# Kernel optimization log

Hardware: AMD Instinct MI355X
Metric: run time of the kernel (lower is better)

The kernel has to match this reference:

```python
import jax, jax.numpy as jnp
import numpy as np

DECAY = 0.8
EPS = 1e-05


def setup_inputs() -> dict:
    key = jax.random.key(0)
    k_x, k_e = jax.random.split(key)
    x = jax.random.normal(k_x, (8, 4096, 256), dtype=jnp.float32)
    embed = jax.random.normal(k_e, (8192, 256), dtype=jnp.float32)
    cluster_size = jnp.zeros((8192,), dtype=jnp.float32)
    embed_avg = embed  # buffer initialized as embed.clone()
    return {"x": x, "embed": embed, "cluster_size": cluster_size, "embed_avg": embed_avg}


def reference(x, embed, cluster_size, embed_avg):
    shape = x.shape
    K, d = embed.shape
    flatten = x.reshape(-1, d)  # [N, d]

    dist = -(jnp.sum(flatten * flatten, axis=1, keepdims=True)
             - 2.0 * (flatten @ embed.T)
             + jnp.sum(embed * embed, axis=1)[None, :])  # [N, K]
    embed_ind = jnp.argmax(dist, axis=-1)  # [N]

    quantize = jnp.take(embed, embed_ind, axis=0).reshape(shape)
    embed_ind_out = embed_ind.reshape(shape[:-1])

    # Training-mode EMA update (one_hot sum / one_hot matmul expressed as scatter-adds)
    counts = jnp.zeros((K,), dtype=x.dtype).at[embed_ind].add(1.0)  # embed_onehot.sum(0)
    embed_sum = jnp.zeros((K, d), dtype=x.dtype).at[embed_ind].add(flatten)  # (flatten^T @ onehot)^T

    new_cluster_size = cluster_size * DECAY + counts * (1.0 - DECAY)
    new_embed_avg = embed_avg * DECAY + embed_sum * (1.0 - DECAY)

    smoothed = (new_cluster_size + EPS) / (new_cluster_size.sum() + K * EPS) * new_cluster_size.sum()
    new_embed = new_embed_avg / smoothed[:, None]

    return quantize, embed_ind_out, new_cluster_size, new_embed_avg, new_embed
```

## Files before the change

### kernel.cpp

```cpp
#include <hip/hip_runtime.h>

#define N_ROWS 32768
#define DIM    256
#define KCODES 8192
#define DECAYF 0.8f
#define OMDF   0.2f
#define EPSF   1e-5f

#define Q_OFF    0
#define IND_OFF  8388608
#define CS_OFF   8421376
#define EA_OFF   8429568
#define NE_OFF   10526720


#define WS_E2    0
#define WS_CNT   8192
#define WS_START 16384
#define WS_CUR   24576
#define WS_SUM   40960

typedef _Float16 half8 __attribute__((ext_vector_type(8)));
typedef float floatx16 __attribute__((ext_vector_type(16)));

#define GLOAD16(g, l) __builtin_amdgcn_global_load_lds( \
    (const __attribute__((address_space(1))) void*)(g), \
    (__attribute__((address_space(3))) void*)(l), 16, 0, 0)

#define PREP_ROWS 32
__global__ void prep_all_kernel(const float* __restrict__ x,
                                const float* __restrict__ embed,
                                const float* __restrict__ cs,
                                _Float16* __restrict__ Xp,
                                _Float16* __restrict__ Ep,
                                float* __restrict__ out,
                                float* __restrict__ ws) {
  __shared__ __align__(16) _Float16 L[PREP_ROWS][264];
  __shared__ float red[4];
  const int t = threadIdx.x;
  const int bid = blockIdx.x;

  if (bid < 1024) {
    if (bid < 128) {
      unsigned long long* gbest = (unsigned long long*)(out + EA_OFF);
      gbest[bid * 256 + t] = 0ULL;
    } else if (bid < 160) {
      ((int*)(ws + WS_CNT))[(bid - 128) * 256 + t] = 0;
    }
    const int row0 = bid * PREP_ROWS;
    #pragma unroll
    for (int it = 0; it < 8; ++it) {
      int idx = it * 256 + t;
      int r = idx >> 6, q = idx & 63;
      float4 v = *(const float4*)&x[(size_t)(row0 + r) * DIM + q * 4];
      L[r][q * 4 + 0] = (_Float16)v.x;
      L[r][q * 4 + 1] = (_Float16)v.y;
      L[r][q * 4 + 2] = (_Float16)v.z;
      L[r][q * 4 + 3] = (_Float16)v.w;
    }
    __syncthreads();
    #pragma unroll
    for (int it = 0; it < 4; ++it) {
      int idx = it * 256 + t;
      int slot = idx >> 5, r = idx & 31;
      *(float4*)&Xp[((size_t)slot * N_ROWS + row0 + r) * 8] =
          *(const float4*)&L[r][slot * 8];
    }
  } else {
    const int row0 = (bid - 1024) * PREP_ROWS;
    float* e2 = ws + WS_E2;
    #pragma unroll
    for (int it = 0; it < 8; ++it) {
      int idx = it * 256 + t;
      int r = idx >> 6, q = idx & 63;
      float4 v = *(const float4*)&embed[(size_t)(row0 + r) * DIM + q * 4];
      L[r][q * 4 + 0] = (_Float16)v.x;
      L[r][q * 4 + 1] = (_Float16)v.y;
      L[r][q * 4 + 2] = (_Float16)v.z;
      L[r][q * 4 + 3] = (_Float16)v.w;
      float ssq = v.x * v.x + v.y * v.y + v.z * v.z + v.w * v.w;
      #pragma unroll
      for (int o = 32; o; o >>= 1) ssq += __shfl_xor(ssq, o);
      if ((t & 63) == 0) e2[row0 + r] = ssq;
    }
    if (bid == 1024) {
      float s = 0.0f;
      for (int j = t; j < KCODES; j += 256) s += cs[j];
      #pragma unroll
      for (int o = 32; o; o >>= 1) s += __shfl_xor(s, o);
      if ((t & 63) == 0) red[t >> 6] = s;
    }
    __syncthreads();
    if (bid == 1024 && t == 0)
      ws[WS_SUM] = red[0] + red[1] + red[2] + red[3];
    #pragma unroll
    for (int it = 0; it < 4; ++it) {
      int idx = it * 256 + t;
      int slot = idx >> 5, r = idx & 31;
      *(float4*)&Ep[((size_t)slot * KCODES + row0 + r) * 8] =
          *(const float4*)&L[r][slot * 8];
    }
  }
}

__global__ __launch_bounds__(512, 2) void main_kernel(
    const _Float16* __restrict__ Xp, const _Float16* __restrict__ Ep,
    const float* __restrict__ e2, unsigned long long* __restrict__ gbest) {
  __shared__ __align__(16) _Float16 As[4 * 4 * 256 * 8];
  __shared__ __align__(16) _Float16 Bs[4 * 4 * 256 * 8];
  __shared__ __align__(16) float e2s[256];

  const int t = threadIdx.x;
  const int w = t >> 6;
  const int lane = t & 63;
  const int l31 = lane & 31;
  const int h = lane >> 5;
  const int wm = w >> 2;
  const int wn = w & 3;

  const int bid = blockIdx.x;
  const int bi = bid >> 3;
  const int cb = (bid & 7) * 4 + (bi >> 3);
  const int rbg = bi & 7;
  const int codes0 = cb * 256;
  const int rowbase = rbg * 4096;

  const bool isA = (w < 4);
  const int slot = isA ? w : (w - 4);

  const _Float16* estage = Ep + ((size_t)slot * KCODES + codes0 + lane) * 8;
  const _Float16* xstage = Xp + ((size_t)slot * N_ROWS + rowbase + lane) * 8;
  _Float16* adst = &As[slot * 2048];
  _Float16* bdst = &Bs[slot * 2048];

  auto stage = [&](int buf, int se4, int rowT) {
    if (isA) {
      const _Float16* src = estage + (size_t)se4 * (KCODES * 8);
      _Float16* dst = adst + buf * 8192;
      #pragma unroll
      for (int q = 0; q < 4; ++q)
        GLOAD16(src + q * 512, dst + q * 512);
    } else {
      const _Float16* src =
          xstage + (size_t)se4 * (N_ROWS * 8) + (size_t)rowT * 2048;
      _Float16* dst = bdst + buf * 8192;
      #pragma unroll
      for (int q = 0; q < 4; ++q)
        GLOAD16(src + q * 512, dst + q * 512);
    }
  };

  if (t < 64) {
    float4 v = *(const float4*)&e2[codes0 + t * 4];
    *(float4*)&e2s[t * 4] = v;
  }
  __builtin_amdgcn_sched_barrier(0);
  stage(0, 0, 0);
  stage(1, 4, 0);
  asm volatile("s_waitcnt vmcnt(4)" ::: "memory");
  asm volatile("s_waitcnt lgkmcnt(0)" ::: "memory");
  __builtin_amdgcn_s_barrier();
  __builtin_amdgcn_sched_barrier(0);

  floatx16 acc[4][2];
  unsigned long long pbest[4][2];

  #pragma unroll 1
  for (int sg = 0; sg < 4; ++sg) {
    #pragma unroll
    for (int tt = 0; tt < 4; ++tt) {
      const int rowT = sg * 4 + tt;
      #pragma unroll
      for (int ct = 0; ct < 4; ++ct) {
        const int cl = wm * 128 + ct * 32 + 4 * h;
        #pragma unroll
        for (int rq = 0; rq < 4; ++rq) {
          float4 v = *(const float4*)&e2s[cl + rq * 8];
          acc[ct][0][rq * 4 + 0] = -0.5f * v.x;
          acc[ct][0][rq * 4 + 1] = -0.5f * v.y;
          acc[ct][0][rq * 4 + 2] = -0.5f * v.z;
          acc[ct][0][rq * 4 + 3] = -0.5f * v.w;
        }
        acc[ct][1] = acc[ct][0];
      }

      #pragma unroll
      for (int i = 0; i < 8; ++i) {
        const bool lastTile = (sg == 3 && tt == 3);
        if (!(lastTile && i >= 6)) {
          const int ip = i + 2;
          stage(ip & 3, (ip & 7) * 4, rowT + (ip >> 3));
        }
        __builtin_amdgcn_sched_barrier(0);

        const int cur = (i & 3) * 8192;
        #pragma unroll
        for (int ks = 0; ks < 2; ++ks) {
          const int sbase = cur + (2 * ks + h) * 2048;
          half8 a0 = *(const half8*)&As[sbase + (wm * 128 + l31) * 8];
          half8 a1 = *(const half8*)&As[sbase + (wm * 128 + 32 + l31) * 8];
          half8 a2 = *(const half8*)&As[sbase + (wm * 128 + 64 + l31) * 8];
          half8 a3 = *(const half8*)&As[sbase + (wm * 128 + 96 + l31) * 8];
          half8 b0 = *(const half8*)&Bs[sbase + (wn * 64 + l31) * 8];
          half8 b1 = *(const half8*)&Bs[sbase + (wn * 64 + 32 + l31) * 8];
          __builtin_amdgcn_s_setprio(1);
          acc[0][0] = __builtin_amdgcn_mfma_f32_32x32x16_f16(a0, b0, acc[0][0], 0, 0, 0);
          acc[0][1] = __builtin_amdgcn_mfma_f32_32x32x16_f16(a0, b1, acc[0][1], 0, 0, 0);
          acc[1][0] = __builtin_amdgcn_mfma_f32_32x32x16_f16(a1, b0, acc[1][0], 0, 0, 0);
          acc[1][1] = __builtin_amdgcn_mfma_f32_32x32x16_f16(a1, b1, acc[1][1], 0, 0, 0);
          acc[2][0] = __builtin_amdgcn_mfma_f32_32x32x16_f16(a2, b0, acc[2][0], 0, 0, 0);
          acc[2][1] = __builtin_amdgcn_mfma_f32_32x32x16_f16(a2, b1, acc[2][1], 0, 0, 0);
          acc[3][0] = __builtin_amdgcn_mfma_f32_32x32x16_f16(a3, b0, acc[3][0], 0, 0, 0);
          acc[3][1] = __builtin_amdgcn_mfma_f32_32x32x16_f16(a3, b1, acc[3][1], 0, 0, 0);
          __builtin_amdgcn_s_setprio(0);
        }
        __builtin_amdgcn_sched_barrier(0);

        if (!(lastTile && i == 7)) {
          if (!(lastTile && i == 6)) {
            asm volatile("s_waitcnt vmcnt(4)" ::: "memory");
          } else {
            asm volatile("s_waitcnt vmcnt(0)" ::: "memory");
          }
          __builtin_amdgcn_s_barrier();
          __builtin_amdgcn_sched_barrier(0);
        }
      }

      #pragma unroll
      for (int rt = 0; rt < 2; ++rt) {
        float best = -3.0e38f;
        int bidx = 0;
        #pragma unroll
        for (int ct = 0; ct < 4; ++ct) {
          const int cbase = codes0 + wm * 128 + ct * 32 + 4 * h;
          #pragma unroll
          for (int r = 0; r < 16; ++r) {
            const int code = cbase + (r & 3) + 8 * (r >> 2);
            float v = acc[ct][rt][r];
            if (v > best || (v == best && code < bidx)) { best = v; bidx = code; }
          }
        }
        unsigned u = __float_as_uint(best);
        u = (u & 0x80000000u) ? ~u : (u | 0x80000000u);
        unsigned long long p =
            ((unsigned long long)u << 32) | (unsigned)(8191 - bidx);
        unsigned long long op = (unsigned long long)__shfl_xor((long long)p, 32);
        if (op > p) p = op;
        pbest[tt][rt] = p;
      }
    }

    #pragma unroll
    for (int tt2 = 0; tt2 < 4; ++tt2)
      #pragma unroll
      for (int rt = 0; rt < 2; ++rt)
        if (h == 0)
          atomicMax(&gbest[rowbase + (sg * 4 + tt2) * 256 + wn * 64 +
                           rt * 32 + l31],
                    pbest[tt2][rt]);
    if (sg < 3) {
      asm volatile("s_waitcnt vmcnt(0)" ::: "memory");
      __builtin_amdgcn_sched_barrier(0);
    }
  }
}

__global__ void decode_count_kernel(const unsigned long long* __restrict__ gbest,
                                    float* __restrict__ out,
                                    int* __restrict__ cnt) {
  int r = blockIdx.x * blockDim.x + threadIdx.x;
  unsigned long long p = gbest[r];
  int k = 8191 - (int)(unsigned)(p & 0xFFFFFFFFull);
  out[IND_OFF + r] = (float)k;
  atomicAdd(&cnt[k], 1);
}

__global__ void prefix_kernel(const int* __restrict__ cnt,
                              int* __restrict__ start,
                              int* __restrict__ cursor) {
  __shared__ int part[1024];
  const int t = threadIdx.x;
  int loc[8];
  int s = 0;
  #pragma unroll
  for (int j = 0; j < 8; ++j) { loc[j] = cnt[t * 8 + j]; s += loc[j]; }
  part[t] = s;
  __syncthreads();
  for (int off = 1; off < 1024; off <<= 1) {
    int v = (t >= off) ? part[t - off] : 0;
    __syncthreads();
    part[t] += v;
    __syncthreads();
  }
  int base = part[t] - s;
  #pragma unroll
  for (int j = 0; j < 8; ++j) {
    start[t * 8 + j] = base;
    cursor[t * 8 + j] = base;
    base += loc[j];
  }
}

__global__ void scatter_rows_kernel(const float* __restrict__ out,
                                    int* __restrict__ cursor,
                                    int* __restrict__ rowlist) {
  int r = blockIdx.x * blockDim.x + threadIdx.x;
  int k = (int)out[IND_OFF + r];
  int pos = atomicAdd(&cursor[k], 1);
  rowlist[pos] = r;
}

__global__ void bucket_final_kernel(const float* __restrict__ x,
                                    const float* __restrict__ cs,
                                    const float* __restrict__ embed_avg,
                                    const int* __restrict__ start,
                                    const int* __restrict__ cnt,
                                    const int* __restrict__ rowlist,
                                    float* __restrict__ out,
                                    const float* __restrict__ ws_sum) {
  const int lane = threadIdx.x & 63;
  const int k = blockIdx.x * 4 + (threadIdx.x >> 6);
  const int s = start[k];
  const int n = cnt[k];
  float4 acc = make_float4(0.f, 0.f, 0.f, 0.f);
  int i = 0;
  for (; i + 2 <= n; i += 2) {
    int r0 = rowlist[s + i];
    int r1 = rowlist[s + i + 1];
    float4 v0 = *(const float4*)&x[(size_t)r0 * DIM + lane * 4];
    float4 v1 = *(const float4*)&x[(size_t)r1 * DIM + lane * 4];
    acc.x += v0.x + v1.x; acc.y += v0.y + v1.y;
    acc.z += v0.z + v1.z; acc.w += v0.w + v1.w;
  }
  if (i < n) {
    int r0 = rowlist[s + i];
    float4 v0 = *(const float4*)&x[(size_t)r0 * DIM + lane * 4];
    acc.x += v0.x; acc.y += v0.y; acc.z += v0.z; acc.w += v0.w;
  }
  const float S = DECAYF * (*ws_sum) + OMDF * (float)N_ROWS;
  const float scale = S / (S + (float)KCODES * EPSF);
  float ncs = cs[k] * DECAYF + (float)n * OMDF;
  if (lane == 0) out[CS_OFF + k] = ncs;
  float4 ea = *(const float4*)&embed_avg[(size_t)k * DIM + lane * 4];
  float4 nea;
  nea.x = ea.x * DECAYF + acc.x * OMDF;
  nea.y = ea.y * DECAYF + acc.y * OMDF;
  nea.z = ea.z * DECAYF + acc.z * OMDF;
  nea.w = ea.w * DECAYF + acc.w * OMDF;
  *(float4*)&out[EA_OFF + (size_t)k * DIM + lane * 4] = nea;
  float inv_sm = 1.0f / ((ncs + EPSF) * scale);
  float4 ne;
  ne.x = nea.x * inv_sm;
  ne.y = nea.y * inv_sm;
  ne.z = nea.z * inv_sm;
  ne.w = nea.w * inv_sm;
  *(float4*)&out[NE_OFF + (size_t)k * DIM + lane * 4] = ne;
}

__global__ void finish_q_kernel(const float* __restrict__ embed,
                                float* __restrict__ out) {
  const int lane = threadIdx.x & 63;
  const int wave = (blockIdx.x * blockDim.x + threadIdx.x) >> 6;
  for (int row = wave; row < N_ROWS; row += 2048) {
    int k = (int)out[IND_OFF + row];
    float4 ev = *(const float4*)&embed[(size_t)k * DIM + lane * 4];
    *(float4*)&out[Q_OFF + (size_t)row * DIM + lane * 4] = ev;
  }
}

extern "C" void kernel_launch(void* const* d_in, const int* in_sizes, int n_in,
                              void* d_out, int out_size, void* d_ws, size_t ws_size,
                              hipStream_t stream) {
  const float* x = (const float*)d_in[0];
  const float* embed = (const float*)d_in[1];
  const float* cs = (const float*)d_in[2];
  const float* ea = (const float*)d_in[3];
  float* out = (float*)d_out;
  float* ws = (float*)d_ws;

  float* e2 = ws + WS_E2;
  int* cnt = (int*)(ws + WS_CNT);
  int* start = (int*)(ws + WS_START);
  int* cursor = (int*)(ws + WS_CUR);
  float* ws_sum = ws + WS_SUM;

  _Float16* Xp = (_Float16*)(out + Q_OFF);
  int* rowlist = (int*)(out + Q_OFF + 4194304);
  unsigned long long* gbest = (unsigned long long*)(out + EA_OFF);
  _Float16* Ep = (_Float16*)(out + EA_OFF + 65536);

  prep_all_kernel<<<1280, 256, 0, stream>>>(x, embed, cs, Xp, Ep, out, ws);
  main_kernel<<<256, 512, 0, stream>>>(Xp, Ep, e2, gbest);
  decode_count_kernel<<<128, 256, 0, stream>>>(gbest, out, cnt);
  prefix_kernel<<<1, 1024, 0, stream>>>(cnt, start, cursor);
  scatter_rows_kernel<<<128, 256, 0, stream>>>(out, cursor, rowlist);
  bucket_final_kernel<<<2048, 256, 0, stream>>>(x, cs, ea, start, cnt,
                                                rowlist, out, ws_sum);
  finish_q_kernel<<<512, 256, 0, stream>>>(embed, out);
}
```

Baseline: 379.1 us.

## Switch main GEMM to 16x16x32 MFMA with split-phase staging and barriers

```diff
diff --git a/kernel.cpp b/kernel.cpp
--- a/kernel.cpp
+++ b/kernel.cpp
@@ -21,7 +21,7 @@
 #define WS_SUM   40960
 
 typedef _Float16 half8 __attribute__((ext_vector_type(8)));
-typedef float floatx16 __attribute__((ext_vector_type(16)));
+typedef float floatx4 __attribute__((ext_vector_type(4)));
 
 #define GLOAD16(g, l) __builtin_amdgcn_global_load_lds( \
     (const __attribute__((address_space(1))) void*)(g), \
@@ -113,8 +113,8 @@
   const int t = threadIdx.x;
   const int w = t >> 6;
   const int lane = t & 63;
-  const int l31 = lane & 31;
-  const int h = lane >> 5;
+  const int l15 = lane & 15;
+  const int g4 = lane >> 4;
   const int wm = w >> 2;
   const int wn = w & 3;
 
@@ -133,20 +133,18 @@
   _Float16* adst = &As[slot * 2048];
   _Float16* bdst = &Bs[slot * 2048];
 
-  auto stage = [&](int buf, int se4, int rowT) {
+  auto stage2 = [&](int buf, int se4, int rowT, int q0) {
     if (isA) {
       const _Float16* src = estage + (size_t)se4 * (KCODES * 8);
       _Float16* dst = adst + buf * 8192;
-      #pragma unroll
-      for (int q = 0; q < 4; ++q)
-        GLOAD16(src + q * 512, dst + q * 512);
+      GLOAD16(src + q0 * 512, dst + q0 * 512);
+      GLOAD16(src + (q0 + 1) * 512, dst + (q0 + 1) * 512);
     } else {
       const _Float16* src =
           xstage + (size_t)se4 * (N_ROWS * 8) + (size_t)rowT * 2048;
       _Float16* dst = bdst + buf * 8192;
-      #pragma unroll
-      for (int q = 0; q < 4; ++q)
-        GLOAD16(src + q * 512, dst + q * 512);
+      GLOAD16(src + q0 * 512, dst + q0 * 512);
+      GLOAD16(src + (q0 + 1) * 512, dst + (q0 + 1) * 512);
     }
   };
 
@@ -155,15 +153,14 @@
     *(float4*)&e2s[t * 4] = v;
   }
   __builtin_amdgcn_sched_barrier(0);
-  stage(0, 0, 0);
-  stage(1, 4, 0);
+  stage2(0, 0, 0, 0); stage2(0, 0, 0, 2);
+  stage2(1, 4, 0, 0); stage2(1, 4, 0, 2);
   asm volatile("s_waitcnt vmcnt(4)" ::: "memory");
   asm volatile("s_waitcnt lgkmcnt(0)" ::: "memory");
   __builtin_amdgcn_s_barrier();
   __builtin_amdgcn_sched_barrier(0);
 
-  floatx16 acc[4][2];
-  unsigned long long pbest[4][2];
+  floatx4 acc[8][4];
 
   #pragma unroll 1
   for (int sg = 0; sg < 4; ++sg) {
@@ -171,51 +168,66 @@
     for (int tt = 0; tt < 4; ++tt) {
       const int rowT = sg * 4 + tt;
       #pragma unroll
-      for (int ct = 0; ct < 4; ++ct) {
-        const int cl = wm * 128 + ct * 32 + 4 * h;
-        #pragma unroll
-        for (int rq = 0; rq < 4; ++rq) {
-          float4 v = *(const float4*)&e2s[cl + rq * 8];
-          acc[ct][0][rq * 4 + 0] = -0.5f * v.x;
-          acc[ct][0][rq * 4 + 1] = -0.5f * v.y;
-          acc[ct][0][rq * 4 + 2] = -0.5f * v.z;
-          acc[ct][0][rq * 4 + 3] = -0.5f * v.w;
-        }
-        acc[ct][1] = acc[ct][0];
+      for (int mf = 0; mf < 8; ++mf) {
+        float4 v = *(const float4*)&e2s[wm * 128 + mf * 16 + g4 * 4];
+        floatx4 a;
+        a[0] = -0.5f * v.x; a[1] = -0.5f * v.y;
+        a[2] = -0.5f * v.z; a[3] = -0.5f * v.w;
+        acc[mf][0] = a; acc[mf][1] = a; acc[mf][2] = a; acc[mf][3] = a;
       }
+      __builtin_amdgcn_sched_barrier(0);
 
       #pragma unroll
       for (int i = 0; i < 8; ++i) {
-        const bool lastTile = (sg == 3 && tt == 3);
-        if (!(lastTile && i >= 6)) {
-          const int ip = i + 2;
-          stage(ip & 3, (ip & 7) * 4, rowT + (ip >> 3));
-        }
-        __builtin_amdgcn_sched_barrier(0);
-
-        const int cur = (i & 3) * 8192;
-        #pragma unroll
-        for (int ks = 0; ks < 2; ++ks) {
-          const int sbase = cur + (2 * ks + h) * 2048;
-          half8 a0 = *(const half8*)&As[sbase + (wm * 128 + l31) * 8];
-          half8 a1 = *(const half8*)&As[sbase + (wm * 128 + 32 + l31) * 8];
-          half8 a2 = *(const half8*)&As[sbase + (wm * 128 + 64 + l31) * 8];
-          half8 a3 = *(const half8*)&As[sbase + (wm * 128 + 96 + l31) * 8];
-          half8 b0 = *(const half8*)&Bs[sbase + (wn * 64 + l31) * 8];
-          half8 b1 = *(const half8*)&Bs[sbase + (wn * 64 + 32 + l31) * 8];
-          __builtin_amdgcn_s_setprio(1);
-          acc[0][0] = __builtin_amdgcn_mfma_f32_32x32x16_f16(a0, b0, acc[0][0], 0, 0, 0);
-          acc[0][1] = __builtin_amdgcn_mfma_f32_32x32x16_f16(a0, b1, acc[0][1], 0, 0, 0);
-          acc[1][0] = __builtin_amdgcn_mfma_f32_32x32x16_f16(a1, b0, acc[1][0], 0, 0, 0);
-          acc[1][1] = __builtin_amdgcn_mfma_f32_32x32x16_f16(a1, b1, acc[1][1], 0, 0, 0);
-          acc[2][0] = __builtin_amdgcn_mfma_f32_32x32x16_f16(a2, b0, acc[2][0], 0, 0, 0);
-          acc[2][1] = __builtin_amdgcn_mfma_f32_32x32x16_f16(a2, b1, acc[2][1], 0, 0, 0);
-          acc[3][0] = __builtin_amdgcn_mfma_f32_32x32x16_f16(a3, b0, acc[3][0], 0, 0, 0);
-          acc[3][1] = __builtin_amdgcn_mfma_f32_32x32x16_f16(a3, b1, acc[3][1], 0, 0, 0);
-          __builtin_amdgcn_s_setprio(0);
-        }
-        __builtin_amdgcn_sched_barrier(0);
-
+        const bool lastTile = (sg == 3) && (tt == 3);
+        const bool doStage = !(lastTile && i >= 6);
+        const int buf = i & 3;
+        const int abase = buf * 8192 + g4 * 2048 + (wm * 128 + l15) * 8;
+        const int bbase = buf * 8192 + g4 * 2048 + (wn * 64 + l15) * 8;
+        const int sbuf = (i + 2) & 3;
+        const int sse4 = ((i + 2) & 7) * 4;
+        const int srow = rowT + ((i + 2) >> 3);
+
+        half8 bf[4], af[4];
+        #pragma unroll
+        for (int nf = 0; nf < 4; ++nf)
+          bf[nf] = *(const half8*)&Bs[bbase + nf * 128];
+        #pragma unroll
+        for (int mf = 0; mf < 4; ++mf)
+          af[mf] = *(const half8*)&As[abase + mf * 128];
+        if (doStage) stage2(sbuf, sse4, srow, 0);
+        __builtin_amdgcn_sched_barrier(0);
+        __builtin_amdgcn_s_barrier();
+        asm volatile("s_waitcnt lgkmcnt(0)" ::: "memory");
+        __builtin_amdgcn_sched_barrier(0);
+        __builtin_amdgcn_s_setprio(1);
+        #pragma unroll
+        for (int mf = 0; mf < 4; ++mf)
+          #pragma unroll
+          for (int nf = 0; nf < 4; ++nf)
+            acc[mf][nf] = __builtin_amdgcn_mfma_f32_16x16x32_f16(
+                af[mf], bf[nf], acc[mf][nf], 0, 0, 0);
+        __builtin_amdgcn_s_setprio(0);
+        __builtin_amdgcn_sched_barrier(0);
+        __builtin_amdgcn_s_barrier();
+
+        #pragma unroll
+        for (int mf = 0; mf < 4; ++mf)
+          af[mf] = *(const half8*)&As[abase + (64 + mf * 16) * 8];
+        if (doStage) stage2(sbuf, sse4, srow, 2);
+        __builtin_amdgcn_sched_barrier(0);
+        __builtin_amdgcn_s_barrier();
+        asm volatile("s_waitcnt lgkmcnt(0)" ::: "memory");
+        __builtin_amdgcn_sched_barrier(0);
+        __builtin_amdgcn_s_setprio(1);
+        #pragma unroll
+        for (int mf = 0; mf < 4; ++mf)
+          #pragma unroll
+          for (int nf = 0; nf < 4; ++nf)
+            acc[4 + mf][nf] = __builtin_amdgcn_mfma_f32_16x16x32_f16(
+                af[mf], bf[nf], acc[4 + mf][nf], 0, 0, 0);
+        __builtin_amdgcn_s_setprio(0);
+        __builtin_amdgcn_sched_barrier(0);
         if (!(lastTile && i == 7)) {
           if (!(lastTile && i == 6)) {
             asm volatile("s_waitcnt vmcnt(4)" ::: "memory");
@@ -223,21 +235,21 @@
             asm volatile("s_waitcnt vmcnt(0)" ::: "memory");
           }
           __builtin_amdgcn_s_barrier();
-          __builtin_amdgcn_sched_barrier(0);
         }
+        __builtin_amdgcn_sched_barrier(0);
       }
 
       #pragma unroll
-      for (int rt = 0; rt < 2; ++rt) {
+      for (int nf = 0; nf < 4; ++nf) {
         float best = -3.0e38f;
         int bidx = 0;
         #pragma unroll
-        for (int ct = 0; ct < 4; ++ct) {
-          const int cbase = codes0 + wm * 128 + ct * 32 + 4 * h;
+        for (int mf = 0; mf < 8; ++mf) {
+          const int cbase = codes0 + wm * 128 + mf * 16 + g4 * 4;
           #pragma unroll
-          for (int r = 0; r < 16; ++r) {
-            const int code = cbase + (r & 3) + 8 * (r >> 2);
-            float v = acc[ct][rt][r];
+          for (int r = 0; r < 4; ++r) {
+            float v = acc[mf][nf][r];
+            const int code = cbase + r;
             if (v > best || (v == best && code < bidx)) { best = v; bidx = code; }
           }
         }
@@ -245,23 +257,17 @@
         u = (u & 0x80000000u) ? ~u : (u | 0x80000000u);
         unsigned long long p =
             ((unsigned long long)u << 32) | (unsigned)(8191 - bidx);
-        unsigned long long op = (unsigned long long)__shfl_xor((long long)p, 32);
+        unsigned long long op = (unsigned long long)__shfl_xor((long long)p, 16);
         if (op > p) p = op;
-        pbest[tt][rt] = p;
+        op = (unsigned long long)__shfl_xor((long long)p, 32);
+        if (op > p) p = op;
+        if (g4 == 0)
+          atomicMax(&gbest[rowbase + rowT * 256 + wn * 64 + nf * 16 + l15], p);
       }
-    }
-
-    #pragma unroll
-    for (int tt2 = 0; tt2 < 4; ++tt2)
-      #pragma unroll
-      for (int rt = 0; rt < 2; ++rt)
-        if (h == 0)
-          atomicMax(&gbest[rowbase + (sg * 4 + tt2) * 256 + wn * 64 +
-                           rt * 32 + l31],
-                    pbest[tt2][rt]);
-    if (sg < 3) {
-      asm volatile("s_waitcnt vmcnt(0)" ::: "memory");
-      __builtin_amdgcn_sched_barrier(0);
+      if (!(sg == 3 && tt == 3)) {
+        asm volatile("s_waitcnt vmcnt(0)" ::: "memory");
+        __builtin_amdgcn_sched_barrier(0);
+      }
     }
   }
 }
```

After: 460.7 us. 1.22x slower.
